# Performance work log

Measured on AMD Instinct MI355X. Metric: run time of the kernel, lower is better.

## Reference

```python
import jax, jax.numpy as jnp
import numpy as np

RENDER_SIZE = 256   # renderer image_size
IMG_H, IMG_W = 480, 640
ORIG_SIZE = 640     # max(H, W)
SIGMA = 0.5         # soft-silhouette sharpness in pixels (approximates NR hard rasterizer)
CHUNK = 128         # faces per scan step (bounds peak memory)
N_VERTS = 2048
N_FACES = 4096


def _se3_exp(dof):
    """dof = [v(3), omega(3)] (pytorch3d order) -> (R [3,3], t [3]) column convention."""
    v, w = dof[:3], dof[3:]
    th2 = jnp.sum(w * w)
    th = jnp.sqrt(th2 + 1e-30)
    small = th < 1e-4
    th_s = jnp.where(small, 1.0, th)          # safe denom (avoids nan grads)
    th2_s = jnp.where(small, 1.0, th2)
    A = jnp.where(small, 1.0 - th2 / 6.0, jnp.sin(th_s) / th_s)
    B = jnp.where(small, 0.5 - th2 / 24.0, (1.0 - jnp.cos(th_s)) / th2_s)
    C = jnp.where(small, 1.0 / 6.0 - th2 / 120.0, (th_s - jnp.sin(th_s)) / (th2_s * th_s))
    Kx = jnp.array([[0.0, -w[2], w[1]], [w[2], 0.0, -w[0]], [-w[1], w[0], 0.0]], dtype=dof.dtype)
    K2 = Kx @ Kx
    I = jnp.eye(3, dtype=dof.dtype)
    R = I + A * Kx + B * K2
    V = I + B * Kx + C * K2   # left Jacobian
    return R, V @ v


def _cross2(u, w):
    return u[..., 0] * w[..., 1] - u[..., 1] * w[..., 0]


def _rasterize_silhouette(tri):
    """tri: [F,3,2] projected triangle verts in render-pixel coords -> [R,R] coverage."""
    P = RENDER_SIZE * RENDER_SIZE
    ys, xs = jnp.meshgrid(jnp.arange(RENDER_SIZE, dtype=jnp.float32) + 0.5,
                          jnp.arange(RENDER_SIZE, dtype=jnp.float32) + 0.5, indexing='ij')
    px, py = xs.reshape(-1), ys.reshape(-1)  # [P] pixel centers
    tris = tri.reshape(N_FACES // CHUNK, CHUNK, 3, 2)

    def body(logp, t3):
        a = t3                          # [C,3,2] edge start verts
        e = jnp.roll(t3, -1, axis=1) - a  # [C,3,2] edge vectors (v1-v0, v2-v1, v0-v2)
        area2 = _cross2(e[:, 0], -e[:, 2])            # signed doubled area, [C]
        sgn = jnp.where(area2 >= 0, 1.0, -1.0)        # winding fix so inside > 0
        elen = jnp.sqrt(jnp.sum(e * e, -1)) + 1e-9    # [C,3]
        c0 = e[..., 0] * a[..., 1] - e[..., 1] * a[..., 0]  # [C,3]
        # signed distance of each pixel to each edge line: [P,C,3]
        d = (e[None, :, :, 0] * py[:, None, None] - e[None, :, :, 1] * px[:, None, None] - c0[None]) / elen[None]
        d = sgn[None, :, None] * d
        dmin = jnp.min(d, axis=2)                     # [P,C] min edge distance
        s = jnp.minimum(jax.nn.sigmoid(dmin / SIGMA), 1.0 - 1e-6)
        return logp + jnp.sum(jnp.log1p(-s), axis=1), None

    logp, _ = jax.lax.scan(body, jnp.zeros(P, jnp.float32), tris)
    return (1.0 - jnp.exp(logp)).reshape(RENDER_SIZE, RENDER_SIZE)


def _resize_nearest(img, size):
    return jax.image.resize(img, (size, size), method='nearest')


def reference(dof, vertices, faces, K, mask_gt):
    R, t = _se3_exp(dof)
    cam = vertices @ R.T + t              # [N,3] camera coords
    uvw = cam @ K.T                       # pinhole projection
    xy = uvw[:, :2] / uvw[:, 2:3]         # pixel coords at orig_size resolution
    xy = xy * (RENDER_SIZE / ORIG_SIZE)   # scale to render grid
    tri = xy[faces]                       # [F,3,2]
    si = _rasterize_silhouette(tri)       # [R,R]
    si = _resize_nearest(si, ORIG_SIZE)[:IMG_H, :IMG_W]
    loss = jnp.sum((si - mask_gt) ** 2)
    return loss, si


def setup_inputs() -> dict:
    key = jax.random.key(0)
    k1, k2, k3, k4 = jax.random.split(key, 4)
    v = jax.random.normal(k1, (N_VERTS, 3), dtype=jnp.float32)
    vertices = 0.5 * v / (jnp.linalg.norm(v, axis=1, keepdims=True) + 1e-8)  # unit-ish sphere mesh
    faces = jax.random.randint(k2, (N_FACES, 3), 0, N_VERTS, dtype=jnp.int32)
    # pose: object ~2.5m in front of camera, small rotation + noise
    dof = jnp.array([0.0, 0.0, 2.5, 0.2, -0.1, 0.15], dtype=jnp.float32) \
          + 0.05 * jax.random.normal(k3, (6,), dtype=jnp.float32)
    K = jnp.array([[600.0, 0.0, 320.0], [0.0, 600.0, 240.0], [0.0, 0.0, 1.0]], dtype=jnp.float32)
    mask_gt = (jax.random.uniform(k4, (IMG_H, IMG_W)) < 0.3).astype(jnp.float32)
    return {"dof": dof, "vertices": vertices, "faces": faces, "K": K, "mask_gt": mask_gt}
```

## Files before the change

### kernel.cpp

```cpp
#include <hip/hip_runtime.h>
#include <math.h>

#define RENDER 256
#define IMG_H 480
#define IMG_W 640
#define NV 2048
#define NF 4096
#define FACE_SLICES 16
#define FACES_PER_SLICE (NF / FACE_SLICES)
#define TILES_X 16
#define TILES_Y_LIVE 12
#define TILES_LIVE (TILES_X * TILES_Y_LIVE)
#define N_UNITS (TILES_LIVE * FACE_SLICES)
#define UNIT_HASH 2053

#define SIGMA_INV 2.0f
#define CAP 13.815510557964274f
#define LOG2E 1.4426950408889634f
#define ZK 2.8853900817779268f
#define CAP2 19.931568569324174f
#define ECAP 999999.0f
#define SKIP_PIX -26.0f

#define WS_FD_OFF    0
#define WS_LOGP_OFF  (192 * 1024)

__global__ __launch_bounds__(256) void k_prep(const float* __restrict__ dof,
                                              const float* __restrict__ verts,
                                              const int* __restrict__ faces,
                                              const float* __restrict__ Km,
                                              float* __restrict__ fdata,
                                              float* __restrict__ logp,
                                              float* __restrict__ out) {
    if (blockIdx.x >= 16) {
        logp[(blockIdx.x - 16) * 256 + threadIdx.x] = 0.0f;
        if (blockIdx.x == 16 && threadIdx.x == 0) out[0] = 0.0f;
        return;
    }

    __shared__ float sxy[NV * 2];

    float v0 = dof[0], v1 = dof[1], v2 = dof[2];
    float w0 = dof[3], w1 = dof[4], w2 = dof[5];
    float th2 = w0 * w0 + w1 * w1 + w2 * w2;
    float th = sqrtf(th2 + 1e-30f);
    bool small = th < 1e-4f;
    float th_s = small ? 1.0f : th;
    float th2_s = small ? 1.0f : th2;
    float A = small ? (1.0f - th2 / 6.0f) : (sinf(th_s) / th_s);
    float B = small ? (0.5f - th2 / 24.0f) : ((1.0f - cosf(th_s)) / th2_s);
    float C = small ? (1.0f / 6.0f - th2 / 120.0f)
                    : ((th_s - sinf(th_s)) / (th2_s * th_s));
    float Kx[9] = {0.0f, -w2, w1, w2, 0.0f, -w0, -w1, w0, 0.0f};
    float w[3] = {w0, w1, w2};
    float R[9], V[9];
    for (int i = 0; i < 3; i++)
        for (int j = 0; j < 3; j++) {
            float K2 = w[i] * w[j] - (i == j ? th2 : 0.0f);
            float id = (i == j) ? 1.0f : 0.0f;
            R[i * 3 + j] = id + A * Kx[i * 3 + j] + B * K2;
            V[i * 3 + j] = id + B * Kx[i * 3 + j] + C * K2;
        }
    float t0 = V[0] * v0 + V[1] * v1 + V[2] * v2;
    float t1 = V[3] * v0 + V[4] * v1 + V[5] * v2;
    float t2 = V[6] * v0 + V[7] * v1 + V[8] * v2;
    float K00 = Km[0], K01 = Km[1], K02 = Km[2];
    float K10 = Km[3], K11 = Km[4], K12 = Km[5];
    float K20 = Km[6], K21 = Km[7], K22 = Km[8];
    const float scale = 256.0f / 640.0f;

    for (int n = threadIdx.x; n < NV; n += 256) {
        float vx = verts[n * 3], vy = verts[n * 3 + 1], vz = verts[n * 3 + 2];
        float cx = R[0] * vx + R[1] * vy + R[2] * vz + t0;
        float cy = R[3] * vx + R[4] * vy + R[5] * vz + t1;
        float cz = R[6] * vx + R[7] * vy + R[8] * vz + t2;
        float u = K00 * cx + K01 * cy + K02 * cz;
        float v = K10 * cx + K11 * cy + K12 * cz;
        float ww = K20 * cx + K21 * cy + K22 * cz;
        float rw = __builtin_amdgcn_rcpf(ww) * scale;
        sxy[n * 2]     = u * rw;
        sxy[n * 2 + 1] = v * rw;
    }
    __syncthreads();

    int f = blockIdx.x * 256 + threadIdx.x;
    int i0 = faces[f * 3], i1 = faces[f * 3 + 1], i2 = faces[f * 3 + 2];
    float x0 = sxy[i0 * 2], y0 = sxy[i0 * 2 + 1];
    float x1 = sxy[i1 * 2], y1 = sxy[i1 * 2 + 1];
    float x2 = sxy[i2 * 2], y2 = sxy[i2 * 2 + 1];
    float ex[3] = {x1 - x0, x2 - x1, x0 - x2};
    float ey[3] = {y1 - y0, y2 - y1, y0 - y2};
    float ax[3] = {x0, x1, x2};
    float ay[3] = {y0, y1, y2};
    float area2 = ex[0] * (-ey[2]) - ey[0] * (-ex[2]);
    float sgn = (area2 >= 0.0f) ? 1.0f : -1.0f;
    float* o = fdata + f * 12;
    for (int k = 0; k < 3; k++) {
        float elen = sqrtf(ex[k] * ex[k] + ey[k] * ey[k]) + 1e-9f;
        float c0 = ex[k] * ay[k] - ey[k] * ax[k];
        float inv = sgn / elen * ZK;
        float Ac = ex[k] * inv;
        float Bc = -ey[k] * inv;
        o[k * 4 + 0] = Ac;
        o[k * 4 + 1] = Bc;
        o[k * 4 + 2] = -c0 * inv;
        o[k * 4 + 3] = 7.5f * (fabsf(Ac) + fabsf(Bc));
    }
}

__global__ __launch_bounds__(256) void k_raster(const float* __restrict__ fdata,
                                                float* __restrict__ logp) {
    __shared__ float s_data[4096];
    __shared__ int s_n;
    __shared__ int s_ncap;
    const int tid = threadIdx.x;
    if (tid == 0) { s_n = 0; s_ncap = 0; }
    __syncthreads();

    const int unit = (int)((blockIdx.x * UNIT_HASH) % N_UNITS);
    const int tile = unit >> 4;
    const int slice = unit & 15;
    const int tileX = tile & 15;
    const int tileY = tile >> 4;
    const float cx = tileX * 16 + 8.0f;
    const float cy = tileY * 16 + 8.0f;
    const float4* __restrict__ fd4 = (const float4*)fdata;

    {
        int f = slice * FACES_PER_SLICE + tid;
        float4 e0 = fd4[f * 3 + 0];
        float4 e1 = fd4[f * 3 + 1];
        float4 e2 = fd4[f * 3 + 2];
        float d0 = fmaf(e0.y, cx, fmaf(e0.x, cy, e0.z));
        float d1 = fmaf(e1.y, cx, fmaf(e1.x, cy, e1.z));
        float d2 = fmaf(e2.y, cx, fmaf(e2.x, cy, e2.z));
        float capm = fminf(d0 - e0.w, fminf(d1 - e1.w, d2 - e2.w));
        float skpm = fminf(d0 + e0.w, fminf(d1 + e1.w, d2 + e2.w));
        bool capped = capm > CAP2;
        bool live = (!capped) && (skpm > SKIP_PIX);
        unsigned long long mcap = __ballot(capped);
        unsigned long long mliv = __ballot(live);
        int lane = tid & 63;
        int base = 0;
        if (lane == 0) {
            base = atomicAdd(&s_n, __popcll(mliv));
            if (mcap) atomicAdd(&s_ncap, __popcll(mcap));
        }
        base = __shfl(base, 0, 64);
        if (live) {
            int pos = base + __popcll(mliv & ((1ull << lane) - 1ull));
            float4* dst = (float4*)(s_data + pos * 12);
            dst[0] = e0; dst[1] = e1; dst[2] = e2;
        }
    }
    __syncthreads();

    const int n = s_n;
    const int ncap = s_ncap;
    if (n == 0 && ncap == 0) return;

    const int wv = tid >> 6;
    const int lane = tid & 63;
    const int row = lane >> 2;
    const int col0 = lane & 3;
    const float py = (float)(tileY * 16 + row) + 0.5f;
    const float px0 = (float)(tileX * 16 + col0) + 0.5f;

    float pm[4] = {1.0f, 1.0f, 1.0f, 1.0f};
    int   pe[4] = {0, 0, 0, 0};
    const float4* sd = (const float4*)s_data;
    if (wv < n) {
        float4 c0 = sd[wv * 3 + 0], c1 = sd[wv * 3 + 1], c2 = sd[wv * 3 + 2];
        int it = 0;
        for (int i = wv; i < n; i += 4) {
            float4 n0 = sd[(i + 4) * 3 + 0];
            float4 n1 = sd[(i + 4) * 3 + 1];
            float4 n2 = sd[(i + 4) * 3 + 2];
            float t0p = fmaf(c0.x, py, c0.z);
            float t1p = fmaf(c1.x, py, c1.z);
            float t2p = fmaf(c2.x, py, c2.z);
            #pragma unroll
            for (int k = 0; k < 4; ++k) {
                float px = px0 + (float)(4 * k);
                float z = fminf(fmaf(c0.y, px, t0p),
                          fminf(fmaf(c1.y, px, t1p), fmaf(c2.y, px, t2p)));
                float e = fminf(__builtin_amdgcn_exp2f(z), ECAP);
                pm[k] = fmaf(pm[k], e, pm[k]);
            }
            if (((++it) & 3) == 0) {
                #pragma unroll
                for (int k = 0; k < 4; ++k) {
                    unsigned b = __float_as_uint(pm[k]);
                    pe[k] += (int)(b >> 23) - 127;
                    pm[k] = __uint_as_float((b & 0x007fffffu) | 0x3f800000u);
                }
            }
            c0 = n0; c1 = n1; c2 = n2;
        }
    }
    float acc[4];
    #pragma unroll
    for (int k = 0; k < 4; ++k)
        acc[k] = -((float)pe[k] + __builtin_amdgcn_logf(pm[k]));

    __syncthreads();
    {
        int base = wv * 1024 + row * 16 + col0;
        s_data[base + 0]  = acc[0];
        s_data[base + 4]  = acc[1];
        s_data[base + 8]  = acc[2];
        s_data[base + 12] = acc[3];
    }
    __syncthreads();
    {
        int p = tid;
        float v = s_data[p] + s_data[1024 + p] + s_data[2048 + p] +
                  s_data[3072 + p] - CAP2 * (float)ncap;
        int iyp = tileY * 16 + (p >> 4);
        int ixp = tileX * 16 + (p & 15);
        atomicAdd(&logp[iyp * RENDER + ixp], v);
    }
}

__global__ __launch_bounds__(256) void k_final(const float* __restrict__ logp,
                                               const float* __restrict__ mask,
                                               float* __restrict__ out) {
    int idx = blockIdx.x * 256 + threadIdx.x;
    int r = idx / IMG_W;
    int c = idx - r * IMG_W;
    int ir = (2 * r + 1) / 5;
    int ic = (2 * c + 1) / 5;
    float si = 1.0f - __builtin_amdgcn_exp2f(logp[ir * RENDER + ic]);
    out[1 + idx] = si;
    float diff = si - mask[idx];
    float d2 = diff * diff;
    #pragma unroll
    for (int off = 32; off > 0; off >>= 1) d2 += __shfl_down(d2, off, 64);
    __shared__ float sred[4];
    int lane = threadIdx.x & 63;
    int wv = threadIdx.x >> 6;
    if (lane == 0) sred[wv] = d2;
    __syncthreads();
    if (threadIdx.x == 0)
        atomicAdd(out, sred[0] + sred[1] + sred[2] + sred[3]);
}

extern "C" void kernel_launch(void* const* d_in, const int* in_sizes, int n_in,
                              void* d_out, int out_size, void* d_ws, size_t ws_size,
                              hipStream_t stream) {
    const float* dof   = (const float*)d_in[0];
    const float* verts = (const float*)d_in[1];
    const int*   faces = (const int*)d_in[2];
    const float* Km    = (const float*)d_in[3];
    const float* mask  = (const float*)d_in[4];
    float* out = (float*)d_out;

    char* ws = (char*)d_ws;
    float* fdata = (float*)(ws + WS_FD_OFF);
    float* logp  = (float*)(ws + WS_LOGP_OFF);

    k_prep<<<16 + TILES_LIVE, 256, 0, stream>>>(dof, verts, faces, Km, fdata, logp, out);
    k_raster<<<N_UNITS, 256, 0, stream>>>(fdata, logp);
    k_final<<<(IMG_H * IMG_W) / 256, 256, 0, stream>>>(logp, mask, out);
}
```

Before: 106.1 us.

## Fuse final resize/loss into raster kernel via last-slice-done counter per tile

Measured after the change: 271.7 us. 2.56x slower.

```diff
diff --git a/kernel.cpp b/kernel.cpp
--- a/kernel.cpp
+++ b/kernel.cpp
@@ -24,6 +24,7 @@
 
 #define WS_FD_OFF    0
 #define WS_LOGP_OFF  (192 * 1024)
+#define WS_DONE_OFF  (448 * 1024)
 
 __global__ __launch_bounds__(256) void k_prep(const float* __restrict__ dof,
                                               const float* __restrict__ verts,
@@ -31,10 +32,14 @@
                                               const float* __restrict__ Km,
                                               float* __restrict__ fdata,
                                               float* __restrict__ logp,
+                                              int* __restrict__ done,
                                               float* __restrict__ out) {
     if (blockIdx.x >= 16) {
         logp[(blockIdx.x - 16) * 256 + threadIdx.x] = 0.0f;
-        if (blockIdx.x == 16 && threadIdx.x == 0) out[0] = 0.0f;
+        if (blockIdx.x == 16) {
+            if (threadIdx.x == 0) out[0] = 0.0f;
+            if (threadIdx.x < TILES_LIVE) done[threadIdx.x] = 0;
+        }
         return;
     }
 
@@ -109,10 +114,16 @@
 }
 
 __global__ __launch_bounds__(256) void k_raster(const float* __restrict__ fdata,
-                                                float* __restrict__ logp) {
+                                                float* __restrict__ logp,
+                                                int* __restrict__ done,
+                                                const float* __restrict__ mask,
+                                                float* __restrict__ out) {
     __shared__ float s_data[4096];
+    __shared__ float s_si[256];
+    __shared__ float s_red[4];
     __shared__ int s_n;
     __shared__ int s_ncap;
+    __shared__ int s_last;
     const int tid = threadIdx.x;
     if (tid == 0) { s_n = 0; s_ncap = 0; }
     __syncthreads();
@@ -125,6 +136,7 @@
     const float cx = tileX * 16 + 8.0f;
     const float cy = tileY * 16 + 8.0f;
     const float4* __restrict__ fd4 = (const float4*)fdata;
+    const int lane = tid & 63;
 
     {
         int f = slice * FACES_PER_SLICE + tid;
@@ -140,7 +152,6 @@
         bool live = (!capped) && (skpm > SKIP_PIX);
         unsigned long long mcap = __ballot(capped);
         unsigned long long mliv = __ballot(live);
-        int lane = tid & 63;
         int base = 0;
         if (lane == 0) {
             base = atomicAdd(&s_n, __popcll(mliv));
@@ -157,92 +168,106 @@
 
     const int n = s_n;
     const int ncap = s_ncap;
-    if (n == 0 && ncap == 0) return;
-
     const int wv = tid >> 6;
-    const int lane = tid & 63;
     const int row = lane >> 2;
     const int col0 = lane & 3;
-    const float py = (float)(tileY * 16 + row) + 0.5f;
-    const float px0 = (float)(tileX * 16 + col0) + 0.5f;
-
-    float pm[4] = {1.0f, 1.0f, 1.0f, 1.0f};
-    int   pe[4] = {0, 0, 0, 0};
-    const float4* sd = (const float4*)s_data;
-    if (wv < n) {
-        float4 c0 = sd[wv * 3 + 0], c1 = sd[wv * 3 + 1], c2 = sd[wv * 3 + 2];
-        int it = 0;
-        for (int i = wv; i < n; i += 4) {
-            float4 n0 = sd[(i + 4) * 3 + 0];
-            float4 n1 = sd[(i + 4) * 3 + 1];
-            float4 n2 = sd[(i + 4) * 3 + 2];
-            float t0p = fmaf(c0.x, py, c0.z);
-            float t1p = fmaf(c1.x, py, c1.z);
-            float t2p = fmaf(c2.x, py, c2.z);
-            #pragma unroll
-            for (int k = 0; k < 4; ++k) {
-                float px = px0 + (float)(4 * k);
-                float z = fminf(fmaf(c0.y, px, t0p),
-                          fminf(fmaf(c1.y, px, t1p), fmaf(c2.y, px, t2p)));
-                float e = fminf(__builtin_amdgcn_exp2f(z), ECAP);
-                pm[k] = fmaf(pm[k], e, pm[k]);
-            }
-            if (((++it) & 3) == 0) {
+
+    if (n != 0 || ncap != 0) {
+        const float py = (float)(tileY * 16 + row) + 0.5f;
+        const float px0 = (float)(tileX * 16 + col0) + 0.5f;
+
+        float pm[4] = {1.0f, 1.0f, 1.0f, 1.0f};
+        int   pe[4] = {0, 0, 0, 0};
+        const float4* sd = (const float4*)s_data;
+        if (wv < n) {
+            float4 c0 = sd[wv * 3 + 0], c1 = sd[wv * 3 + 1], c2 = sd[wv * 3 + 2];
+            int it = 0;
+            for (int i = wv; i < n; i += 4) {
+                float4 n0 = sd[(i + 4) * 3 + 0];
+                float4 n1 = sd[(i + 4) * 3 + 1];
+                float4 n2 = sd[(i + 4) * 3 + 2];
+                float t0p = fmaf(c0.x, py, c0.z);
+                float t1p = fmaf(c1.x, py, c1.z);
+                float t2p = fmaf(c2.x, py, c2.z);
                 #pragma unroll
                 for (int k = 0; k < 4; ++k) {
-                    unsigned b = __float_as_uint(pm[k]);
-                    pe[k] += (int)(b >> 23) - 127;
-                    pm[k] = __uint_as_float((b & 0x007fffffu) | 0x3f800000u);
+                    float px = px0 + (float)(4 * k);
+                    float z = fminf(fmaf(c0.y, px, t0p),
+                              fminf(fmaf(c1.y, px, t1p), fmaf(c2.y, px, t2p)));
+                    float e = fminf(__builtin_amdgcn_exp2f(z), ECAP);
+                    pm[k] = fmaf(pm[k], e, pm[k]);
                 }
+                if (((++it) & 3) == 0) {
+                    #pragma unroll
+                    for (int k = 0; k < 4; ++k) {
+                        unsigned b = __float_as_uint(pm[k]);
+                        pe[k] += (int)(b >> 23) - 127;
+                        pm[k] = __uint_as_float((b & 0x007fffffu) | 0x3f800000u);
+                    }
+                }
+                c0 = n0; c1 = n1; c2 = n2;
             }
-            c0 = n0; c1 = n1; c2 = n2;
-        }
-    }
-    float acc[4];
-    #pragma unroll
-    for (int k = 0; k < 4; ++k)
-        acc[k] = -((float)pe[k] + __builtin_amdgcn_logf(pm[k]));
-
-    __syncthreads();
-    {
-        int base = wv * 1024 + row * 16 + col0;
-        s_data[base + 0]  = acc[0];
-        s_data[base + 4]  = acc[1];
-        s_data[base + 8]  = acc[2];
-        s_data[base + 12] = acc[3];
-    }
-    __syncthreads();
-    {
-        int p = tid;
-        float v = s_data[p] + s_data[1024 + p] + s_data[2048 + p] +
-                  s_data[3072 + p] - CAP2 * (float)ncap;
-        int iyp = tileY * 16 + (p >> 4);
-        int ixp = tileX * 16 + (p & 15);
-        atomicAdd(&logp[iyp * RENDER + ixp], v);
-    }
-}
-
-__global__ __launch_bounds__(256) void k_final(const float* __restrict__ logp,
-                                               const float* __restrict__ mask,
-                                               float* __restrict__ out) {
-    int idx = blockIdx.x * 256 + threadIdx.x;
-    int r = idx / IMG_W;
-    int c = idx - r * IMG_W;
-    int ir = (2 * r + 1) / 5;
-    int ic = (2 * c + 1) / 5;
-    float si = 1.0f - __builtin_amdgcn_exp2f(logp[ir * RENDER + ic]);
-    out[1 + idx] = si;
-    float diff = si - mask[idx];
-    float d2 = diff * diff;
-    #pragma unroll
-    for (int off = 32; off > 0; off >>= 1) d2 += __shfl_down(d2, off, 64);
-    __shared__ float sred[4];
-    int lane = threadIdx.x & 63;
-    int wv = threadIdx.x >> 6;
-    if (lane == 0) sred[wv] = d2;
-    __syncthreads();
-    if (threadIdx.x == 0)
-        atomicAdd(out, sred[0] + sred[1] + sred[2] + sred[3]);
+        }
+        float acc[4];
+        #pragma unroll
+        for (int k = 0; k < 4; ++k)
+            acc[k] = -((float)pe[k] + __builtin_amdgcn_logf(pm[k]));
+
+        __syncthreads();
+        {
+            int base = wv * 1024 + row * 16 + col0;
+            s_data[base + 0]  = acc[0];
+            s_data[base + 4]  = acc[1];
+            s_data[base + 8]  = acc[2];
+            s_data[base + 12] = acc[3];
+        }
+        __syncthreads();
+        {
+            int p = tid;
+            float v = s_data[p] + s_data[1024 + p] + s_data[2048 + p] +
+                      s_data[3072 + p] - CAP2 * (float)ncap;
+            int iyp = tileY * 16 + (p >> 4);
+            int ixp = tileX * 16 + (p & 15);
+            atomicAdd(&logp[iyp * RENDER + ixp], v);
+        }
+    }
+
+    __threadfence();
+    __syncthreads();
+    if (tid == 0)
+        s_last = (atomicAdd(&done[tile], 1) == FACE_SLICES - 1) ? 1 : 0;
+    __syncthreads();
+
+    if (s_last) {
+        __threadfence();
+        {
+            int p = tid;
+            int iyp = tileY * 16 + (p >> 4);
+            int ixp = tileX * 16 + (p & 15);
+            float lp = atomicAdd(&logp[iyp * RENDER + ixp], 0.0f);
+            s_si[p] = 1.0f - __builtin_amdgcn_exp2f(lp);
+        }
+        __syncthreads();
+        float d2 = 0.0f;
+        for (int q = tid; q < 1600; q += 256) {
+            int ro = q / 40, co = q - ro * 40;
+            int Rr = tileY * 40 + ro;
+            int Cc = tileX * 40 + co;
+            int ir = (2 * Rr + 1) / 5;
+            int ic = (2 * Cc + 1) / 5;
+            float si = s_si[(ir & 15) * 16 + (ic & 15)];
+            int idx = Rr * IMG_W + Cc;
+            out[1 + idx] = si;
+            float df = si - mask[idx];
+            d2 = fmaf(df, df, d2);
+        }
+        #pragma unroll
+        for (int off = 32; off > 0; off >>= 1) d2 += __shfl_down(d2, off, 64);
+        if (lane == 0) s_red[wv] = d2;
+        __syncthreads();
+        if (tid == 0)
+            atomicAdd(out, s_red[0] + s_red[1] + s_red[2] + s_red[3]);
+    }
 }
 
 extern "C" void kernel_launch(void* const* d_in, const int* in_sizes, int n_in,
@@ -258,8 +283,9 @@
     char* ws = (char*)d_ws;
     float* fdata = (float*)(ws + WS_FD_OFF);
     float* logp  = (float*)(ws + WS_LOGP_OFF);
-
-    k_prep<<<16 + TILES_LIVE, 256, 0, stream>>>(dof, verts, faces, Km, fdata, logp, out);
-    k_raster<<<N_UNITS, 256, 0, stream>>>(fdata, logp);
-    k_final<<<(IMG_H * IMG_W) / 256, 256, 0, stream>>>(logp, mask, out);
+    int*   done  = (int*)(ws + WS_DONE_OFF);
+
+    k_prep<<<16 + TILES_LIVE, 256, 0, stream>>>(dof, verts, faces, Km,
+                                                fdata, logp, done, out);
+    k_raster<<<N_UNITS, 256, 0, stream>>>(fdata, logp, done, mask, out);
 }
```
